# Optimization experiments

Measured on AMD Instinct MI355X. Metric: run time of the kernel, lower is better.

Reference implementation:

```python
import jax, jax.numpy as jnp
import numpy as np

GROUPS = 32
EPS = 1e-5


def conv1x1(x, w, b):
    # x: [B,C,T], w: [O,C], b: [O]
    return jnp.einsum('bct,oc->bot', x, w) + b[None, :, None]


def group_norm(x, g, be):
    B, C, T = x.shape
    xg = x.reshape(B, GROUPS, C // GROUPS, T)
    mean = xg.mean(axis=(2, 3), keepdims=True)
    var = xg.var(axis=(2, 3), keepdims=True)
    xg = (xg - mean) * jax.lax.rsqrt(var + EPS)
    return xg.reshape(B, C, T) * g[None, :, None] + be[None, :, None]


def block(x, w, b, g, be):
    return jax.nn.relu(group_norm(conv1x1(x, w, b), g, be))


def _build_table(x, L):
    # sparse table for range-max: tabs[k][..., t] = max(x[..., t : t+2^k]) (clamped)
    T = x.shape[-1]
    tabs = [x]
    for k in range(1, L + 1):
        step = 1 << (k - 1)
        idx = jnp.minimum(jnp.arange(T) + step, T - 1)
        tabs.append(jnp.maximum(tabs[-1], tabs[-1][..., idx]))
    return jnp.stack(tabs)  # [L+1, B, C, T]


def _range_max_query(S, s, e):
    # S: [L+1,B,C,T]; s,e: [B,N] inclusive range -> [B,C,N]
    length = jnp.maximum(e - s + 1, 1)
    k = jnp.floor(jnp.log2(length.astype(jnp.float32))).astype(jnp.int32)
    e2 = jnp.maximum(e - jnp.left_shift(1, k) + 1, 0)

    def per_b(Sb, kb, sb, eb):
        # Sb: [L+1,C,T]; returns [N,C]
        return jnp.maximum(Sb[kb, :, sb], Sb[kb, :, eb])

    out = jax.vmap(per_b, in_axes=(1, 0, 0, 0))(S, k, s, e2)  # [B,N,C]
    return out.transpose(0, 2, 1)


def boundary_max_pooling(x, segments):
    # x: [B,C,T]; segments: [B,N,4] float boundaries -> [B,C,N]
    B, C, T = x.shape
    s = jnp.clip(jnp.floor(segments).astype(jnp.int32), 0, T - 1)
    e = jnp.clip(jnp.ceil(segments).astype(jnp.int32), 0, T - 1)
    L = max(1, int(np.ceil(np.log2(T))))
    half = C // 2
    S = _build_table(x, L)
    left = _range_max_query(S[:, :, :half], s[..., 0], jnp.maximum(e[..., 1], s[..., 0]))
    right = _range_max_query(S[:, :, half:], s[..., 2], jnp.maximum(e[..., 3], s[..., 2]))
    return jnp.concatenate([left, right], axis=1)


def setup_inputs() -> dict:
    key = jax.random.key(0)
    ks = jax.random.split(key, 12)
    B, Cin, pc, T, Tf, N = 4, 512, 256, 2048, 4096, 2048
    f = lambda k, sh: jax.random.normal(k, sh, jnp.float32)

    def segs(k, tmax):
        raw = jax.random.uniform(k, (B, N, 4), jnp.float32, 0.0, tmax - 1.0)
        return jnp.concatenate([jnp.sort(raw[..., :2], -1), jnp.sort(raw[..., 2:], -1)], -1)

    return {
        'feature': f(ks[0], (B, Cin, T)),
        'frame_level_feature': f(ks[1], (B, pc, Tf)),
        'segments': segs(ks[2], T),
        'frame_segments': segs(ks[3], Tf),
        'feature_lastclass': f(ks[4], (B, 250, N)),
        'ConfResult_feature': f(ks[5], (B, 250, N)),
        'w_cur': f(ks[6], (pc, Cin)) * 0.02, 'b_cur': jnp.zeros((pc,)),
        'g_cur': jnp.ones((pc,)), 'be_cur': jnp.zeros((pc,)),
        'w_lr': f(ks[7], (2 * pc, Cin)) * 0.02, 'b_lr': jnp.zeros((2 * pc,)),
        'g_lr': jnp.ones((2 * pc,)), 'be_lr': jnp.zeros((2 * pc,)),
        'w_roi': f(ks[8], (pc, pc)) * 0.02, 'b_roi': jnp.zeros((pc,)),
        'g_roi': jnp.ones((pc,)), 'be_roi': jnp.zeros((pc,)),
        'w_prop': f(ks[9], (Cin, 4 * pc + 500)) * 0.02, 'b_prop': jnp.zeros((Cin,)),
        'g_prop': jnp.ones((Cin,)), 'be_prop': jnp.zeros((Cin,)),
    }


def reference(feature, frame_level_feature, segments, frame_segments,
              feature_lastclass, ConfResult_feature,
              w_cur, b_cur, g_cur, be_cur,
              w_lr, b_lr, g_lr, be_lr,
              w_roi, b_roi, g_roi, be_roi,
              w_prop, b_prop, g_prop, be_prop):
    fm_short = block(feature, w_cur, b_cur, g_cur, be_cur)          # [B,pc,T]
    feat = block(feature, w_lr, b_lr, g_lr, be_lr)                  # [B,2pc,T]
    prop_feature = boundary_max_pooling(feat, segments)             # [B,2pc,N]
    prop_roi = boundary_max_pooling(frame_level_feature, frame_segments)  # [B,pc,N]
    prop_roi = block(prop_roi, w_roi, b_roi, g_roi, be_roi)
    cat = jnp.concatenate([prop_roi, prop_feature, fm_short,
                           feature_lastclass, ConfResult_feature], axis=1)  # [B,4pc+500,N]
    out = block(cat, w_prop, b_prop, g_prop, be_prop)               # [B,Cin,N]
    return (out, feat)
```

## Files before the change

kernel.cpp:

```cpp
#include <hip/hip_runtime.h>
#include <hip/hip_bf16.h>

#define GROUPS 32
#define EPS_GN 1e-5f

typedef short bf16x8 __attribute__((ext_vector_type(8)));
typedef float f32x4 __attribute__((ext_vector_type(4)));

__device__ __forceinline__ ushort to_bf16_bits(float v) {
  __hip_bfloat16 h = __float2bfloat16(v);
  return *(ushort*)&h;
}
__device__ __forceinline__ float bflo(unsigned u) { return __uint_as_float(u << 16); }
__device__ __forceinline__ float bfhi(unsigned u) { return __uint_as_float(u & 0xffff0000u); }
__device__ __forceinline__ ushort bfpack(float f) {
  return (ushort)(__float_as_uint(f) >> 16);
}

__global__ __launch_bounds__(256)
void cast_w_kernel(const float* __restrict__ w, ushort* __restrict__ wb,
                   int K, int Kp, int total)
{
  int idx = blockIdx.x * 256 + threadIdx.x;
  if (idx >= total) return;
  int o = idx / Kp, k = idx - o * Kp;
  float v = (k < K) ? w[(size_t)o * K + k] : 0.f;
  wb[idx] = to_bf16_bits(v);
}

__global__ __launch_bounds__(256)
void transpose_cast_off(const float* __restrict__ src, ushort* __restrict__ dst,
                        int C, int T, int dstride, int coff, int Cpad)
{
  __shared__ float tile[32][33];
  const int b = blockIdx.z;
  const int c0 = blockIdx.y * 32, t0 = blockIdx.x * 32;
  const int tx = threadIdx.x & 31, ty = threadIdx.x >> 5;
#pragma unroll
  for (int i = 0; i < 4; ++i) {
    const int c = c0 + ty + 8 * i;
    tile[ty + 8 * i][tx] = (c < C) ? src[((size_t)b * C + c) * T + t0 + tx] : 0.f;
  }
  __syncthreads();
  const int cw = c0 + tx;
  if (cw >= Cpad) return;
#pragma unroll
  for (int i = 0; i < 4; ++i)
    dst[((size_t)b * T + t0 + ty + 8 * i) * dstride + coff + cw] =
        to_bf16_bits(tile[tx][ty + 8 * i]);
}

__global__ __launch_bounds__(256)
void bmxt_kernel(const ushort* __restrict__ xt, ushort* __restrict__ bx,
                 int C, int T, int TB, int total8)
{
  int idx = blockIdx.x * 256 + threadIdx.x;
  if (idx >= total8) return;
  const int nc8 = C >> 3;
  const int ci = idx % nc8;
  const int rt = idx / nc8;
  const int tb = rt % TB, b = rt / TB;
  const ushort* p = xt + ((size_t)b * T + (size_t)tb * 32) * C + ci * 8;
  float m[8];
#pragma unroll
  for (int i = 0; i < 8; ++i) m[i] = -3.402823466e38f;
  for (int j = 0; j < 32; ++j) {
    const uint4 v = *(const uint4*)(p + (size_t)j * C);
    m[0] = fmaxf(m[0], bflo(v.x)); m[1] = fmaxf(m[1], bfhi(v.x));
    m[2] = fmaxf(m[2], bflo(v.y)); m[3] = fmaxf(m[3], bfhi(v.y));
    m[4] = fmaxf(m[4], bflo(v.z)); m[5] = fmaxf(m[5], bfhi(v.z));
    m[6] = fmaxf(m[6], bflo(v.w)); m[7] = fmaxf(m[7], bfhi(v.w));
  }
  uint4 o;
  o.x = (unsigned)bfpack(m[0]) | ((unsigned)bfpack(m[1]) << 16);
  o.y = (unsigned)bfpack(m[2]) | ((unsigned)bfpack(m[3]) << 16);
  o.z = (unsigned)bfpack(m[4]) | ((unsigned)bfpack(m[5]) << 16);
  o.w = (unsigned)bfpack(m[6]) | ((unsigned)bfpack(m[7]) << 16);
  *(uint4*)(bx + (size_t)rt * C + ci * 8) = o;
}

template<int CHL>
__global__ __launch_bounds__(256)
void pool_t_kernel(const ushort* __restrict__ xt, const ushort* __restrict__ bx,
                   const float* __restrict__ segs, ushort* __restrict__ dst,
                   int C, int T, int TB, int N, int dstride, int coff)
{
  const int b    = blockIdx.z;
  const int half = blockIdx.y;
  const int n    = blockIdx.x * 4 + (threadIdx.x >> 6);
  const int lane = threadIdx.x & 63;
  const int c    = half * (C >> 1) + lane * CHL;

  const float4 sg = *(const float4*)(segs + ((size_t)b * N + n) * 4);
  const float f0 = half ? sg.z : sg.x;
  const float f1 = half ? sg.w : sg.y;
  int s = min(max((int)floorf(f0), 0), T - 1);
  int e = min(max((int)ceilf(f1), 0), T - 1);
  e = max(e, s);

  const ushort* xp = xt + (size_t)b * T * C + c;
  const ushort* bp = bx + (size_t)b * TB * C + c;
  float m[CHL];
#pragma unroll
  for (int i = 0; i < CHL; ++i) m[i] = -3.402823466e38f;

  auto acc = [&](const ushort* p) {
    if constexpr (CHL == 4) {
      const uint2 v = *(const uint2*)p;
      m[0] = fmaxf(m[0], bflo(v.x)); m[1] = fmaxf(m[1], bfhi(v.x));
      m[2] = fmaxf(m[2], bflo(v.y)); m[3] = fmaxf(m[3], bfhi(v.y));
    } else {
      const unsigned v = *(const unsigned*)p;
      m[0] = fmaxf(m[0], bflo(v)); m[1] = fmaxf(m[1], bfhi(v));
    }
  };

  const int b0 = s >> 5, b1 = e >> 5;
  if (b0 == b1) {
    for (int t = s; t <= e; ++t) acc(xp + (size_t)t * C);
  } else {
    const int t0e = (b0 + 1) << 5;
    for (int t = s; t < t0e; ++t) acc(xp + (size_t)t * C);
    for (int bb = b0 + 1; bb < b1; ++bb) acc(bp + (size_t)bb * C);
    for (int t = (b1 << 5); t <= e; ++t) acc(xp + (size_t)t * C);
  }

  ushort* op = dst + ((size_t)b * N + n) * dstride + coff + c;
  if constexpr (CHL == 4) {
    uint2 o;
    o.x = (unsigned)bfpack(m[0]) | ((unsigned)bfpack(m[1]) << 16);
    o.y = (unsigned)bfpack(m[2]) | ((unsigned)bfpack(m[3]) << 16);
    *(uint2*)op = o;
  } else {
    *(unsigned*)op = (unsigned)bfpack(m[0]) | ((unsigned)bfpack(m[1]) << 16);
  }
}

__global__ __launch_bounds__(256)
void mfma_gemm(const ushort* __restrict__ Wb, const ushort* __restrict__ Xt,
               const float* __restrict__ bias, float* __restrict__ out,
               int O, int K, int T)
{
  const int b  = blockIdx.z;
  const int o0 = blockIdx.y * 128;
  const int t0 = blockIdx.x * 128;
  const int lane = threadIdx.x & 63;
  const int wid  = threadIdx.x >> 6;
  const int wm = wid >> 1, wn = wid & 1;
  const int lr = lane & 15;
  const int lq = lane >> 4;

  const ushort* wp = Wb + (size_t)(o0 + wm * 64 + lr) * K + lq * 8;
  const ushort* xp = Xt + ((size_t)b * T + t0 + wn * 64 + lr) * K + lq * 8;

  f32x4 acc[4][4];
#pragma unroll
  for (int i = 0; i < 4; ++i)
#pragma unroll
    for (int j = 0; j < 4; ++j) acc[i][j] = (f32x4){0.f, 0.f, 0.f, 0.f};

  for (int k0 = 0; k0 < K; k0 += 32) {
    bf16x8 a[4], bt[4];
#pragma unroll
    for (int i = 0; i < 4; ++i)
      a[i] = *(const bf16x8*)(wp + (size_t)i * 16 * K + k0);
#pragma unroll
    for (int j = 0; j < 4; ++j)
      bt[j] = *(const bf16x8*)(xp + (size_t)j * 16 * K + k0);
#pragma unroll
    for (int i = 0; i < 4; ++i)
#pragma unroll
      for (int j = 0; j < 4; ++j)
        acc[i][j] = __builtin_amdgcn_mfma_f32_16x16x32_bf16(a[i], bt[j], acc[i][j], 0, 0, 0);
  }

#pragma unroll
  for (int i = 0; i < 4; ++i) {
#pragma unroll
    for (int r = 0; r < 4; ++r) {
      const int o = o0 + wm * 64 + i * 16 + lq * 4 + r;
      const float bs = bias[o];
      float* op = out + ((size_t)b * O + o) * T + t0 + wn * 64 + lr;
#pragma unroll
      for (int j = 0; j < 4; ++j) op[j * 16] = acc[i][j][r] + bs;
    }
  }
}

__global__ __launch_bounds__(256)
void gn_relu_inplace(float* __restrict__ x, const float* __restrict__ gamma,
                     const float* __restrict__ beta, int C, int Tn, int tshift)
{
  const int b = blockIdx.x / GROUPS;
  const int g = blockIdx.x % GROUPS;
  const int Cg = C / GROUPS;
  const size_t base = ((size_t)b * C + (size_t)g * Cg) * Tn;
  const int M = Cg * Tn;
  const int tid = threadIdx.x;

  float sum = 0.f, ss = 0.f;
  for (int i = tid * 4; i < M; i += 256 * 4) {
    float4 v = *(const float4*)(x + base + i);
    sum += v.x + v.y + v.z + v.w;
    ss  += v.x * v.x + v.y * v.y + v.z * v.z + v.w * v.w;
  }
#pragma unroll
  for (int off = 32; off > 0; off >>= 1) {
    sum += __shfl_down(sum, off);
    ss  += __shfl_down(ss, off);
  }
  __shared__ float s1[4], s2[4];
  __shared__ float smean, sinv;
  const int wid = tid >> 6, lane = tid & 63;
  if (lane == 0) { s1[wid] = sum; s2[wid] = ss; }
  __syncthreads();
  if (tid == 0) {
    float t1 = s1[0] + s1[1] + s1[2] + s1[3];
    float t2 = s2[0] + s2[1] + s2[2] + s2[3];
    float mean = t1 / (float)M;
    float var  = t2 / (float)M - mean * mean;
    smean = mean;
    sinv  = rsqrtf(var + EPS_GN);
  }
  __syncthreads();
  const float mean = smean, inv = sinv;
  for (int i = tid * 4; i < M; i += 256 * 4) {
    float4 v = *(const float4*)(x + base + i);
    const int ch = g * Cg + (i >> tshift);
    const float sc = gamma[ch] * inv;
    const float sh = beta[ch] - mean * sc;
    v.x = fmaxf(v.x * sc + sh, 0.f);
    v.y = fmaxf(v.y * sc + sh, 0.f);
    v.z = fmaxf(v.z * sc + sh, 0.f);
    v.w = fmaxf(v.w * sc + sh, 0.f);
    *(float4*)(x + base + i) = v;
  }
}

extern "C" void kernel_launch(void* const* d_in, const int* in_sizes, int n_in,
                              void* d_out, int out_size, void* d_ws, size_t ws_size,
                              hipStream_t stream)
{
  (void)in_sizes; (void)n_in; (void)out_size; (void)ws_size;

  const float* feature  = (const float*)d_in[0];
  const float* frame    = (const float*)d_in[1];
  const float* segments = (const float*)d_in[2];
  const float* fsegs    = (const float*)d_in[3];
  const float* flc      = (const float*)d_in[4];
  const float* conf     = (const float*)d_in[5];
  const float* w_cur  = (const float*)d_in[6];
  const float* b_cur  = (const float*)d_in[7];
  const float* g_cur  = (const float*)d_in[8];
  const float* be_cur = (const float*)d_in[9];
  const float* w_lr   = (const float*)d_in[10];
  const float* b_lr   = (const float*)d_in[11];
  const float* g_lr   = (const float*)d_in[12];
  const float* be_lr  = (const float*)d_in[13];
  const float* w_roi  = (const float*)d_in[14];
  const float* b_roi  = (const float*)d_in[15];
  const float* g_roi  = (const float*)d_in[16];
  const float* be_roi = (const float*)d_in[17];
  const float* w_prop = (const float*)d_in[18];
  const float* b_prop = (const float*)d_in[19];
  const float* g_prop = (const float*)d_in[20];
  const float* be_prop= (const float*)d_in[21];

  float* OUT0 = (float*)d_out;
  float* FOUT = (float*)d_out + 4194304;

  float* ws  = (float*)d_ws;
  float* Y1  = ws;
  float* RF  = Y1 + 2097152;
  ushort* U    = (ushort*)(RF + 2097152);
  ushort* FT   = U;
  ushort* FRT  = FT + 4194304;
  ushort* BMXF = FRT + 4194304;
  ushort* BMXR = BMXF + 131072;
  ushort* RPT  = BMXR + 131072;
  ushort* CATT = RPT + 2097152;
  ushort* WCB  = CATT + 12582912;
  ushort* WLB  = WCB + 131072;
  ushort* WRB  = WLB + 262144;
  ushort* WPB  = WRB + 65536;

  cast_w_kernel<<<dim3(512),  256, 0, stream>>>(w_cur,  WCB, 512, 512, 131072);
  cast_w_kernel<<<dim3(1024), 256, 0, stream>>>(w_lr,   WLB, 512, 512, 262144);
  cast_w_kernel<<<dim3(256),  256, 0, stream>>>(w_roi,  WRB, 256, 256, 65536);
  cast_w_kernel<<<dim3(3072), 256, 0, stream>>>(w_prop, WPB, 1524, 1536, 786432);

  transpose_cast_off<<<dim3(64, 16, 4), 256, 0, stream>>>(feature, FT, 512, 2048, 512, 0, 512);

  mfma_gemm<<<dim3(16, 2, 4), 256, 0, stream>>>(WCB, FT, b_cur, Y1, 256, 512, 2048);
  gn_relu_inplace<<<dim3(128), 256, 0, stream>>>(Y1, g_cur, be_cur, 256, 2048, 11);

  mfma_gemm<<<dim3(16, 4, 4), 256, 0, stream>>>(WLB, FT, b_lr, FOUT, 512, 512, 2048);
  gn_relu_inplace<<<dim3(128), 256, 0, stream>>>(FOUT, g_lr, be_lr, 512, 2048, 11);

  transpose_cast_off<<<dim3(64, 16, 4), 256, 0, stream>>>(FOUT, FT, 512, 2048, 512, 0, 512);
  bmxt_kernel<<<dim3(64), 256, 0, stream>>>(FT, BMXF, 512, 2048, 64, 16384);
  pool_t_kernel<4><<<dim3(512, 2, 4), 256, 0, stream>>>(
      FT, BMXF, segments, CATT, 512, 2048, 64, 2048, 1536, 256);

  transpose_cast_off<<<dim3(128, 8, 4), 256, 0, stream>>>(frame, FRT, 256, 4096, 256, 0, 256);
  bmxt_kernel<<<dim3(64), 256, 0, stream>>>(FRT, BMXR, 256, 4096, 128, 16384);
  pool_t_kernel<2><<<dim3(512, 2, 4), 256, 0, stream>>>(
      FRT, BMXR, fsegs, RPT, 256, 4096, 128, 2048, 256, 0);

  mfma_gemm<<<dim3(16, 2, 4), 256, 0, stream>>>(WRB, RPT, b_roi, RF, 256, 256, 2048);
  gn_relu_inplace<<<dim3(128), 256, 0, stream>>>(RF, g_roi, be_roi, 256, 2048, 11);

  transpose_cast_off<<<dim3(64, 8, 4), 256, 0, stream>>>(RF,  CATT, 256, 2048, 1536, 0,    256);
  transpose_cast_off<<<dim3(64, 8, 4), 256, 0, stream>>>(Y1,  CATT, 256, 2048, 1536, 768,  256);
  transpose_cast_off<<<dim3(64, 8, 4), 256, 0, stream>>>(flc, CATT, 250, 2048, 1536, 1024, 250);
  transpose_cast_off<<<dim3(64, 9, 4), 256, 0, stream>>>(conf,CATT, 250, 2048, 1536, 1274, 262);

  mfma_gemm<<<dim3(16, 4, 4), 256, 0, stream>>>(WPB, CATT, b_prop, OUT0, 512, 1536, 2048);
  gn_relu_inplace<<<dim3(128), 256, 0, stream>>>(OUT0, g_prop, be_prop, 512, 2048, 11);
}
```

Before: 482.8 us.

## Add 8-row block-max level and multi-accumulator scans to boundary pooling

Replaces the single 32-row block-max table with a two-level hierarchy (8-row and 32-row maxima, the latter built from the former), so the partial ranges at segment edges are scanned mostly over 8-row maxima instead of individual timesteps. The scan loop also uses four independent max accumulators to expose more memory-level parallelism. This adds an extra reduction kernel per input and more workspace in exchange for fewer loads per segment.

Result: faster. 413.7 us (-14.3%).

```diff
diff --git a/kernel.cpp b/kernel.cpp
--- a/kernel.cpp
+++ b/kernel.cpp
@@ -51,20 +51,19 @@
 }
 
 __global__ __launch_bounds__(256)
-void bmxt_kernel(const ushort* __restrict__ xt, ushort* __restrict__ bx,
-                 int C, int T, int TB, int total8)
+void bmx_reduce(const ushort* __restrict__ src, ushort* __restrict__ dst,
+                int C, int rows, int total8)
 {
   int idx = blockIdx.x * 256 + threadIdx.x;
   if (idx >= total8) return;
   const int nc8 = C >> 3;
   const int ci = idx % nc8;
   const int rt = idx / nc8;
-  const int tb = rt % TB, b = rt / TB;
-  const ushort* p = xt + ((size_t)b * T + (size_t)tb * 32) * C + ci * 8;
+  const ushort* p = src + (size_t)rt * rows * C + ci * 8;
   float m[8];
 #pragma unroll
   for (int i = 0; i < 8; ++i) m[i] = -3.402823466e38f;
-  for (int j = 0; j < 32; ++j) {
+  for (int j = 0; j < rows; ++j) {
     const uint4 v = *(const uint4*)(p + (size_t)j * C);
     m[0] = fmaxf(m[0], bflo(v.x)); m[1] = fmaxf(m[1], bfhi(v.x));
     m[2] = fmaxf(m[2], bflo(v.y)); m[3] = fmaxf(m[3], bfhi(v.y));
@@ -76,14 +75,15 @@
   o.y = (unsigned)bfpack(m[2]) | ((unsigned)bfpack(m[3]) << 16);
   o.z = (unsigned)bfpack(m[4]) | ((unsigned)bfpack(m[5]) << 16);
   o.w = (unsigned)bfpack(m[6]) | ((unsigned)bfpack(m[7]) << 16);
-  *(uint4*)(bx + (size_t)rt * C + ci * 8) = o;
+  *(uint4*)(dst + (size_t)rt * C + ci * 8) = o;
 }
 
 template<int CHL>
 __global__ __launch_bounds__(256)
-void pool_t_kernel(const ushort* __restrict__ xt, const ushort* __restrict__ bx,
-                   const float* __restrict__ segs, ushort* __restrict__ dst,
-                   int C, int T, int TB, int N, int dstride, int coff)
+void pool_t_kernel(const ushort* __restrict__ xt, const ushort* __restrict__ bx32,
+                   const ushort* __restrict__ bx8, const float* __restrict__ segs,
+                   ushort* __restrict__ dst,
+                   int C, int T, int TB32, int TB8, int N, int dstride, int coff)
 {
   const int b    = blockIdx.z;
   const int half = blockIdx.y;
@@ -98,41 +98,66 @@
   int e = min(max((int)ceilf(f1), 0), T - 1);
   e = max(e, s);
 
-  const ushort* xp = xt + (size_t)b * T * C + c;
-  const ushort* bp = bx + (size_t)b * TB * C + c;
-  float m[CHL];
-#pragma unroll
-  for (int i = 0; i < CHL; ++i) m[i] = -3.402823466e38f;
-
-  auto acc = [&](const ushort* p) {
+  const ushort* xp  = xt  + (size_t)b * T    * C + c;
+  const ushort* bp  = bx32+ (size_t)b * TB32 * C + c;
+  const ushort* b8p = bx8 + (size_t)b * TB8  * C + c;
+
+  float m[4][CHL];
+#pragma unroll
+  for (int u = 0; u < 4; ++u)
+#pragma unroll
+    for (int i = 0; i < CHL; ++i) m[u][i] = -3.402823466e38f;
+
+  auto acc1 = [&](float* mm, const ushort* p) {
     if constexpr (CHL == 4) {
       const uint2 v = *(const uint2*)p;
-      m[0] = fmaxf(m[0], bflo(v.x)); m[1] = fmaxf(m[1], bfhi(v.x));
-      m[2] = fmaxf(m[2], bflo(v.y)); m[3] = fmaxf(m[3], bfhi(v.y));
+      mm[0] = fmaxf(mm[0], bflo(v.x)); mm[1] = fmaxf(mm[1], bfhi(v.x));
+      mm[2] = fmaxf(mm[2], bflo(v.y)); mm[3] = fmaxf(mm[3], bfhi(v.y));
     } else {
       const unsigned v = *(const unsigned*)p;
-      m[0] = fmaxf(m[0], bflo(v)); m[1] = fmaxf(m[1], bfhi(v));
+      mm[0] = fmaxf(mm[0], bflo(v)); mm[1] = fmaxf(mm[1], bfhi(v));
     }
   };
+  auto scan = [&](const ushort* p, int cnt) {
+    int i = 0;
+    for (; i + 4 <= cnt; i += 4) {
+      acc1(m[0], p);
+      acc1(m[1], p + (size_t)C);
+      acc1(m[2], p + 2 * (size_t)C);
+      acc1(m[3], p + 3 * (size_t)C);
+      p += 4 * (size_t)C;
+    }
+    for (; i < cnt; ++i) { acc1(m[0], p); p += (size_t)C; }
+  };
 
   const int b0 = s >> 5, b1 = e >> 5;
   if (b0 == b1) {
-    for (int t = s; t <= e; ++t) acc(xp + (size_t)t * C);
+    scan(xp + (size_t)s * C, e - s + 1);
   } else {
     const int t0e = (b0 + 1) << 5;
-    for (int t = s; t < t0e; ++t) acc(xp + (size_t)t * C);
-    for (int bb = b0 + 1; bb < b1; ++bb) acc(bp + (size_t)bb * C);
-    for (int t = (b1 << 5); t <= e; ++t) acc(xp + (size_t)t * C);
-  }
+    const int a8 = (s + 7) & ~7;
+    scan(xp + (size_t)s * C, a8 - s);
+    scan(b8p + (size_t)(a8 >> 3) * C, (t0e - a8) >> 3);
+    scan(bp + (size_t)(b0 + 1) * C, b1 - b0 - 1);
+    const int r0 = b1 << 5;
+    const int cnt8 = ((e + 1) >> 3) - (r0 >> 3);
+    scan(b8p + (size_t)(r0 >> 3) * C, cnt8);
+    const int ts = r0 + (cnt8 << 3);
+    scan(xp + (size_t)ts * C, e - ts + 1);
+  }
+
+#pragma unroll
+  for (int i = 0; i < CHL; ++i)
+    m[0][i] = fmaxf(fmaxf(m[0][i], m[1][i]), fmaxf(m[2][i], m[3][i]));
 
   ushort* op = dst + ((size_t)b * N + n) * dstride + coff + c;
   if constexpr (CHL == 4) {
     uint2 o;
-    o.x = (unsigned)bfpack(m[0]) | ((unsigned)bfpack(m[1]) << 16);
-    o.y = (unsigned)bfpack(m[2]) | ((unsigned)bfpack(m[3]) << 16);
+    o.x = (unsigned)bfpack(m[0][0]) | ((unsigned)bfpack(m[0][1]) << 16);
+    o.y = (unsigned)bfpack(m[0][2]) | ((unsigned)bfpack(m[0][3]) << 16);
     *(uint2*)op = o;
   } else {
-    *(unsigned*)op = (unsigned)bfpack(m[0]) | ((unsigned)bfpack(m[1]) << 16);
+    *(unsigned*)op = (unsigned)bfpack(m[0][0]) | ((unsigned)bfpack(m[0][1]) << 16);
   }
 }
 
@@ -275,9 +300,11 @@
   ushort* U    = (ushort*)(RF + 2097152);
   ushort* FT   = U;
   ushort* FRT  = FT + 4194304;
-  ushort* BMXF = FRT + 4194304;
-  ushort* BMXR = BMXF + 131072;
-  ushort* RPT  = BMXR + 131072;
+  ushort* BX8F = FRT + 4194304;
+  ushort* BX32F= BX8F + 524288;
+  ushort* BX8R = BX32F + 131072;
+  ushort* BX32R= BX8R + 524288;
+  ushort* RPT  = BX32R + 131072;
   ushort* CATT = RPT + 2097152;
   ushort* WCB  = CATT + 12582912;
   ushort* WLB  = WCB + 131072;
@@ -298,14 +325,16 @@
   gn_relu_inplace<<<dim3(128), 256, 0, stream>>>(FOUT, g_lr, be_lr, 512, 2048, 11);
 
   transpose_cast_off<<<dim3(64, 16, 4), 256, 0, stream>>>(FOUT, FT, 512, 2048, 512, 0, 512);
-  bmxt_kernel<<<dim3(64), 256, 0, stream>>>(FT, BMXF, 512, 2048, 64, 16384);
+  bmx_reduce<<<dim3(256), 256, 0, stream>>>(FT,   BX8F,  512, 8, 65536);
+  bmx_reduce<<<dim3(64),  256, 0, stream>>>(BX8F, BX32F, 512, 4, 16384);
   pool_t_kernel<4><<<dim3(512, 2, 4), 256, 0, stream>>>(
-      FT, BMXF, segments, CATT, 512, 2048, 64, 2048, 1536, 256);
+      FT, BX32F, BX8F, segments, CATT, 512, 2048, 64, 256, 2048, 1536, 256);
 
   transpose_cast_off<<<dim3(128, 8, 4), 256, 0, stream>>>(frame, FRT, 256, 4096, 256, 0, 256);
-  bmxt_kernel<<<dim3(64), 256, 0, stream>>>(FRT, BMXR, 256, 4096, 128, 16384);
+  bmx_reduce<<<dim3(256), 256, 0, stream>>>(FRT,  BX8R,  256, 8, 65536);
+  bmx_reduce<<<dim3(64),  256, 0, stream>>>(BX8R, BX32R, 256, 4, 16384);
   pool_t_kernel<2><<<dim3(512, 2, 4), 256, 0, stream>>>(
-      FRT, BMXR, fsegs, RPT, 256, 4096, 128, 2048, 256, 0);
+      FRT, BX32R, BX8R, fsegs, RPT, 256, 4096, 128, 512, 2048, 256, 0);
 
   mfma_gemm<<<dim3(16, 2, 4), 256, 0, stream>>>(WRB, RPT, b_roi, RF, 256, 256, 2048);
   gn_relu_inplace<<<dim3(128), 256, 0, stream>>>(RF, g_roi, be_roi, 256, 2048, 11);
```
